# Performance work log

Hardware: AMD Instinct MI355X
Metric: run time of the kernel (lower is better)

The kernel has to match this reference:

```python
import jax, jax.numpy as jnp
import numpy as np

B, LV, LS = 16, 512, 512
FEA_V, FEA_S = 2048, 768
D_MODEL, H, DK, DV = 1024, 16, 64, 64
EPS = 1e-6


def setup_inputs() -> dict:
    key = jax.random.key(0)
    ks = jax.random.split(key, 16)
    sc = lambda fan_in: 1.0 / np.sqrt(fan_in)
    return {
        "v": jax.random.normal(ks[0], (B, LV, FEA_V), jnp.float32),
        "s": jax.random.normal(ks[1], (B, LS, FEA_S), jnp.float32),
        "W_lv": jax.random.normal(ks[2], (FEA_V, D_MODEL), jnp.float32) * sc(FEA_V),
        "b_lv": jnp.zeros((D_MODEL,), jnp.float32),
        "W_ls": jax.random.normal(ks[3], (FEA_S, D_MODEL), jnp.float32) * sc(FEA_S),
        "b_ls": jnp.zeros((D_MODEL,), jnp.float32),
        "pos_v": jax.random.normal(ks[4], (1, LV, D_MODEL), jnp.float32),
        "pos_s": jax.random.normal(ks[5], (1, LS, D_MODEL), jnp.float32),
        "W_q": jax.random.normal(ks[6], (D_MODEL, H * DK), jnp.float32) * sc(D_MODEL),
        "b_q": jnp.zeros((H * DK,), jnp.float32),
        "W_k": jax.random.normal(ks[7], (D_MODEL, H * DK), jnp.float32) * sc(D_MODEL),
        "b_k": jnp.zeros((H * DK,), jnp.float32),
        "W_v": jax.random.normal(ks[8], (D_MODEL, H * DV), jnp.float32) * sc(D_MODEL),
        "b_v": jnp.zeros((H * DV,), jnp.float32),
        "W_p": jax.random.normal(ks[9], (H * DV, D_MODEL), jnp.float32) * sc(H * DV),
        "b_p": jnp.zeros((D_MODEL,), jnp.float32),
        "ln_gamma": jnp.ones((D_MODEL,), jnp.float32),
        "ln_beta": jnp.zeros((D_MODEL,), jnp.float32),
        "v_len": LV,
        "s_len": LS,
    }


def _layer_norm(x, gamma, beta):
    mu = jnp.mean(x, axis=-1, keepdims=True)
    var = jnp.var(x, axis=-1, keepdims=True)
    return gamma * (x - mu) / jnp.sqrt(var + EPS) + beta


def reference(v, s, W_lv, b_lv, W_ls, b_ls, pos_v, pos_s, W_q, b_q, W_k, b_k,
              W_v, b_v, W_p, b_p, ln_gamma, ln_beta, v_len, s_len):
    b_size = v.shape[0]
    # input projections + ReLU (dropout is identity at eval)
    v = jax.nn.relu(v @ W_lv + b_lv)  # [B, LV, D]
    s = jax.nn.relu(s @ W_ls + b_ls)  # [B, LS, D]
    # positional embedding add (pos=True)
    residual_v = v + pos_v[:, : v.shape[1], :]
    # QKV projections; note the original unpack `q_v, k_s, k_s = ...`
    # overwrites the key with the VALUE projection of s, so both key and
    # value in attention are v_s (the W_v projection of s). W_k output is
    # computed in torch but discarded.
    q = (v @ W_q + b_q).reshape(b_size, -1, H, DK).transpose(0, 2, 1, 3)   # [B,H,LV,DK]
    _k = (s @ W_k + b_k)  # computed then discarded, kept for faithfulness
    vs = (s @ W_v + b_v).reshape(b_size, -1, H, DV).transpose(0, 2, 1, 3)  # [B,H,LS,DV]
    scores = jnp.einsum("bhqd,bhkd->bhqk", q, vs) / jnp.sqrt(jnp.float32(DK))
    attn = jax.nn.softmax(scores, axis=-1)
    context = jnp.einsum("bhqk,bhkd->bhqd", attn, vs)  # [B,H,LV,DV]
    context = context.transpose(0, 2, 1, 3).reshape(b_size, -1, H * DV)
    output_v = context @ W_p + b_p  # dropout identity at eval
    return _layer_norm(residual_v + output_v, ln_gamma, ln_beta)
```

## Files before the change

### kernel.cpp

```cpp
#include <hip/hip_runtime.h>

typedef unsigned short u16;
typedef unsigned int   u32;

using bf16x8 = __attribute__((ext_vector_type(8))) short;
using f32x4  = __attribute__((ext_vector_type(4))) float;

#define MFMA16(a, b, c) __builtin_amdgcn_mfma_f32_16x16x32_bf16((a), (b), (c), 0, 0, 0)

__device__ __forceinline__ u16 f2bf(float f) {
  union { float f; u32 u; } x; x.f = f;
  u32 r = x.u + 0x7fffu + ((x.u >> 16) & 1u);
  return (u16)(r >> 16);
}

__device__ __forceinline__ float bf2f(u16 v) {
  union { u32 u; float f; } x; x.u = ((u32)v) << 16;
  return x.f;
}

__device__ __forceinline__ u32 cvtpk(float lo, float hi) {
  u32 r;
  asm("v_cvt_pk_bf16_f32 %0, %1, %2" : "=v"(r) : "v"(lo), "v"(hi));
  return r;
}

__device__ __forceinline__ void gl2lds16(const void* g, void* l) {
  __builtin_amdgcn_global_load_lds(
      (const __attribute__((address_space(1))) u32*)g,
      (__attribute__((address_space(3))) u32*)l, 16, 0, 0);
}

__global__ __launch_bounds__(256) void cvt_all(const float* __restrict__ v_in,
                                               u16* __restrict__ v_bf,
                                               const float* __restrict__ s_in,
                                               u16* __restrict__ s_bf) {
  long i = (long)blockIdx.x * 256 + threadIdx.x;
  const float* in;
  u16* out;
  if (i < 2097152) {
    in = v_in + i * 8;
    out = v_bf + i * 8;
  } else {
    long j = i - 2097152;
    in = s_in + j * 8;
    out = s_bf + j * 8;
  }
  const float4* p = (const float4*)in;
  float4 a = p[0], b = p[1];
  uint4 pk;
  pk.x = cvtpk(a.x, a.y);
  pk.y = cvtpk(a.z, a.w);
  pk.z = cvtpk(b.x, b.y);
  pk.w = cvtpk(b.z, b.w);
  *(uint4*)out = pk;
}

__device__ __forceinline__ void wt_body(const float* __restrict__ W,
                                        u16* __restrict__ Wt, int K, int N,
                                        int bid, u16 (*t)[66]) {
  int tilesN = N >> 6;
  int k0 = (bid / tilesN) << 6;
  int n0 = (bid % tilesN) << 6;
  int tid = threadIdx.x;
  int c4 = (tid & 15) * 4, r16 = tid >> 4;
#pragma unroll
  for (int p = 0; p < 4; ++p) {
    int row = r16 + p * 16;
    float4 f = *(const float4*)(W + (size_t)(k0 + row) * N + n0 + c4);
    t[row][c4 + 0] = f2bf(f.x);
    t[row][c4 + 1] = f2bf(f.y);
    t[row][c4 + 2] = f2bf(f.z);
    t[row][c4 + 3] = f2bf(f.w);
  }
  __syncthreads();
  int c8 = (tid & 7) * 8, r32 = tid >> 3;
#pragma unroll
  for (int p = 0; p < 2; ++p) {
    int n = r32 + p * 32;
    u16 tmp[8] __attribute__((aligned(16)));
#pragma unroll
    for (int e = 0; e < 8; ++e) tmp[e] = t[c8 + e][n];
    *(uint4*)(Wt + (size_t)(n0 + n) * K + k0 + c8) = *(uint4*)tmp;
  }
}

__global__ __launch_bounds__(256) void wt_all(
    const float* W_lv, u16* Wlv_t, const float* W_ls, u16* Wls_t,
    const float* W_q, u16* Wq_t, const float* W_v, u16* Wv_t,
    const float* W_p, u16* Wp_t) {
  __shared__ u16 t[64][66];
  int b = (int)blockIdx.x;
  if (b < 512)        wt_body(W_lv, Wlv_t, 2048, 1024, b, t);
  else if (b < 704)   wt_body(W_ls, Wls_t, 768, 1024, b - 512, t);
  else if (b < 960)   wt_body(W_q, Wq_t, 1024, 1024, b - 704, t);
  else if (b < 1216)  wt_body(W_v, Wv_t, 1024, 1024, b - 960, t);
  else                wt_body(W_p, Wp_t, 1024, 1024, b - 1216, t);
}

struct GArgs {
  const u16* A; const u16* Bt; const float* bias;
  u16* outb; float* outf; u16* outt;
  const u16* add0b; const float* add1;
  int M, N, K;
};

template <int MODE>
__device__ __forceinline__ void gemm_body(u16* sAs, u16* sBs, const GArgs g,
                                          int orig, int nwg) {
  const u16* A = g.A;
  const u16* Bt = g.Bt;
  int N = g.N, K = g.K;
  int tilesN = N >> 7;
  int cpx = nwg >> 3;
  int wg = (orig & 7) * cpx + (orig >> 3);
  int tm = wg / tilesN, tn = wg % tilesN;
  int m0 = tm << 7, n0 = tn << 7;
  int tid = threadIdx.x, w = tid >> 6, l = tid & 63;
  int wm = (w >> 2) << 6, wn = (w & 3) << 5;
  int c16 = l & 15, hi = l >> 4, g16 = hi * 16;

  f32x4 acc[4][2];
#pragma unroll
  for (int i = 0; i < 4; ++i)
#pragma unroll
    for (int j = 0; j < 2; ++j) acc[i][j] = (f32x4){0.f, 0.f, 0.f, 0.f};

  auto STAGE = [&](int kt, int buf) {
    const u16* Ab = A + (size_t)m0 * K + kt * 64;
    const u16* Bb = Bt + (size_t)n0 * K + kt * 64;
#pragma unroll
    for (int p = 0; p < 2; ++p) {
      int lin = p * 8192 + tid * 16;
      int row = lin >> 7;
      int cb = (lin & 127) ^ ((row & 7) << 4);
      int base = lin & ~1023;
      gl2lds16(Ab + (size_t)row * K + (cb >> 1), (char*)sAs + buf * 16384 + base);
      gl2lds16(Bb + (size_t)row * K + (cb >> 1), (char*)sBs + buf * 16384 + base);
    }
  };

  auto COMPUTE = [&](int buf) {
#pragma unroll
    for (int kk = 0; kk < 2; ++kk) {
      bf16x8 af[4], bfr[2];
#pragma unroll
      for (int i = 0; i < 4; ++i) {
        int ar = wm + i * 16 + c16;
        af[i] = *(const bf16x8*)((const char*)sAs + buf * 16384 + ar * 128 +
                                 ((kk * 64 + g16) ^ ((ar & 7) << 4)));
      }
#pragma unroll
      for (int j = 0; j < 2; ++j) {
        int br = wn + j * 16 + c16;
        bfr[j] = *(const bf16x8*)((const char*)sBs + buf * 16384 + br * 128 +
                                  ((kk * 64 + g16) ^ ((br & 7) << 4)));
      }
#pragma unroll
      for (int i = 0; i < 4; ++i)
#pragma unroll
        for (int j = 0; j < 2; ++j) acc[i][j] = MFMA16(af[i], bfr[j], acc[i][j]);
    }
  };

  int nk = K >> 6;
  STAGE(0, 0);
  int cur = 0;
  for (int kt = 0; kt < nk; ++kt) {
    if (kt + 1 < nk) {
      STAGE(kt + 1, cur ^ 1);
      __builtin_amdgcn_sched_barrier(0);
      asm volatile("s_waitcnt vmcnt(4)" ::: "memory");
    } else {
      asm volatile("s_waitcnt vmcnt(0)" ::: "memory");
    }
    __builtin_amdgcn_s_barrier();
    __builtin_amdgcn_sched_barrier(0);
    COMPUTE(cur);
    __builtin_amdgcn_sched_barrier(0);
    __builtin_amdgcn_s_barrier();
    cur ^= 1;
  }

#pragma unroll
  for (int i = 0; i < 4; ++i) {
#pragma unroll
    for (int j = 0; j < 2; ++j) {
      float vv[4];
      int gn = n0 + wn + j * 16 + c16;
#pragma unroll
      for (int r = 0; r < 4; ++r) vv[r] = acc[i][j][r] + g.bias[gn];
      int gm0 = m0 + wm + i * 16 + hi * 4;
      if (MODE == 0) {
#pragma unroll
        for (int r = 0; r < 4; ++r)
          g.outb[(size_t)(gm0 + r) * N + gn] = f2bf(fmaxf(vv[r], 0.f));
      } else if (MODE == 2 || MODE == 4) {
        int hh = gn >> 6, dk = gn & 63, bb2 = gm0 >> 9, ll2 = gm0 & 511;
#pragma unroll
        for (int r = 0; r < 4; ++r)
          g.outb[(((size_t)bb2 * 16 + hh) * 512 + ll2 + r) * 64 + dk] = f2bf(vv[r]);
        if (MODE == 4) {
          uint2 tw;
          tw.x = cvtpk(vv[0], vv[1]);
          tw.y = cvtpk(vv[2], vv[3]);
          *(uint2*)(g.outt + (((size_t)bb2 * 16 + hh) * 64 + dk) * 512 + ll2) = tw;
        }
      } else {
#pragma unroll
        for (int r = 0; r < 4; ++r) {
          int gm = gm0 + r;
          float v = vv[r] + bf2f(g.add0b[(size_t)gm * N + gn]) +
                    g.add1[(size_t)(gm & 511) * N + gn];
          g.outf[(size_t)gm * N + gn] = v;
        }
      }
    }
  }
}

template <int MODEA, int MODEB>
__global__ __launch_bounds__(512) void gemm_pair(GArgs ga, GArgs gb) {
  __shared__ u16 sA[2 * 8192];
  __shared__ u16 sB[2 * 8192];
  int b = (int)blockIdx.x;
  if (b < 512) gemm_body<MODEA>(sA, sB, ga, b, 512);
  else         gemm_body<MODEB>(sA, sB, gb, b - 512, 512);
}

template <int MODE>
__global__ __launch_bounds__(512) void gemm_single(GArgs g) {
  __shared__ u16 sA[2 * 8192];
  __shared__ u16 sB[2 * 8192];
  gemm_body<MODE>(sA, sB, g, (int)blockIdx.x, (int)gridDim.x);
}

__global__ __launch_bounds__(512) void attn_kernel(const u16* __restrict__ q,
                                                   const u16* __restrict__ kv,
                                                   const u16* __restrict__ kvT,
                                                   u16* __restrict__ ctx) {
  __shared__ u16 sK[2][4096];
  __shared__ u16 sVT[2][4096];
  __shared__ u16 sP[8192];

  int orig = (int)blockIdx.x;
  int r = (orig & 7) * 128 + (orig >> 3);
  int bh = r >> 2, qt = r & 3;
  int b = bh >> 4, h = bh & 15;
  int tid = threadIdx.x, w = tid >> 6, l = tid & 63;
  int c16 = l & 15, hi = l >> 4, g16 = hi * 16;
  int swzq = (c16 & 7) << 4;

  const u16* qbase = q + (size_t)bh * 32768 + (size_t)qt * 8192;
#pragma unroll
  for (int j = 0; j < 2; ++j) {
    int chunk = w * 2 + j;
    int lin = chunk * 1024 + l * 16;
    int row = lin >> 7;
    int cb = (lin & 127) ^ ((row & 7) << 4);
    gl2lds16(qbase + (size_t)row * 64 + (cb >> 1), (char*)sP + chunk * 1024);
  }
  {
    const u16* kb = kv + (size_t)bh * 32768;
    const u16* vb = kvT + (size_t)bh * 32768;
    int lin = w * 1024 + l * 16;
    int row = lin >> 7;
    int cb = (lin & 127) ^ ((row & 7) << 4);
    gl2lds16(kb + (size_t)row * 64 + (cb >> 1), (char*)sK[0] + w * 1024);
    gl2lds16(vb + (size_t)row * 512 + (cb >> 1), (char*)sVT[0] + w * 1024);
  }
  __syncthreads();

  const char* sQrow = (const char*)sP + (w * 16 + c16) * 128;
  bf16x8 qf0 = *(const bf16x8*)(sQrow + ((0 + g16) ^ swzq));
  bf16x8 qf1 = *(const bf16x8*)(sQrow + ((64 + g16) ^ swzq));

  char* sPw = (char*)sP + w * 2048;
  f32x4 of[4];
#pragma unroll
  for (int n = 0; n < 4; ++n) of[n] = (f32x4){0.f, 0.f, 0.f, 0.f};
  float m_run = -1e30f, l_run = 0.f;

  for (int c = 0; c < 8; ++c) {
    int cur = c & 1;
    if (c < 7) {
      const u16* kb = kv + (size_t)bh * 32768 + (size_t)(c + 1) * 4096;
      const u16* vb = kvT + (size_t)bh * 32768 + (c + 1) * 64;
      int lin = w * 1024 + l * 16;
      int row = lin >> 7;
      int cb = (lin & 127) ^ ((row & 7) << 4);
      gl2lds16(kb + (size_t)row * 64 + (cb >> 1), (char*)sK[cur ^ 1] + w * 1024);
      gl2lds16(vb + (size_t)row * 512 + (cb >> 1), (char*)sVT[cur ^ 1] + w * 1024);
    }
    const char* kbuf = (const char*)sK[cur];
    const char* vtbuf = (const char*)sVT[cur];

    f32x4 sf[4];
#pragma unroll
    for (int n = 0; n < 4; ++n) {
      const char* krow = kbuf + (n * 16 + c16) * 128;
      bf16x8 k0 = *(const bf16x8*)(krow + (g16 ^ swzq));
      bf16x8 k1 = *(const bf16x8*)(krow + ((64 + g16) ^ swzq));
      f32x4 z = (f32x4){0.f, 0.f, 0.f, 0.f};
      z = MFMA16(k0, qf0, z);
      z = MFMA16(k1, qf1, z);
      sf[n] = z;
    }

    float pmax = -1e30f;
#pragma unroll
    for (int n = 0; n < 4; ++n)
#pragma unroll
      for (int rr = 0; rr < 4; ++rr) {
        sf[n][rr] *= 0.125f;
        pmax = fmaxf(pmax, sf[n][rr]);
      }
    pmax = fmaxf(pmax, __shfl_xor(pmax, 16));
    pmax = fmaxf(pmax, __shfl_xor(pmax, 32));
    float mnew = fmaxf(m_run, pmax);
    float corr = __expf(m_run - mnew);
    float psum = 0.f;
#pragma unroll
    for (int n = 0; n < 4; ++n)
#pragma unroll
      for (int rr = 0; rr < 4; ++rr) {
        float p = __expf(sf[n][rr] - mnew);
        sf[n][rr] = p;
        psum += p;
      }
    psum += __shfl_xor(psum, 16);
    psum += __shfl_xor(psum, 32);
    l_run = l_run * corr + psum;
    m_run = mnew;
#pragma unroll
    for (int n = 0; n < 4; ++n)
#pragma unroll
      for (int rr = 0; rr < 4; ++rr) of[n][rr] *= corr;

#pragma unroll
    for (int n = 0; n < 4; ++n) {
      uint2 pw;
      pw.x = cvtpk(sf[n][0], sf[n][1]);
      pw.y = cvtpk(sf[n][2], sf[n][3]);
      *(uint2*)(sPw + c16 * 128 + ((n * 32 + hi * 8) ^ swzq)) = pw;
    }

    bf16x8 pf0 = *(const bf16x8*)(sPw + c16 * 128 + (g16 ^ swzq));
    bf16x8 pf1 = *(const bf16x8*)(sPw + c16 * 128 + ((64 + g16) ^ swzq));
#pragma unroll
    for (int n = 0; n < 4; ++n) {
      const char* vrow = vtbuf + (n * 16 + c16) * 128;
      bf16x8 v0 = *(const bf16x8*)(vrow + (g16 ^ swzq));
      bf16x8 v1 = *(const bf16x8*)(vrow + ((64 + g16) ^ swzq));
      of[n] = MFMA16(v0, pf0, of[n]);
      of[n] = MFMA16(v1, pf1, of[n]);
    }
    __syncthreads();
  }

  float inv = 1.0f / l_run;
  int grow = qt * 128 + w * 16 + c16;
  u16* obase = ctx + (size_t)(b * 512 + grow) * 1024 + h * 64;
#pragma unroll
  for (int n = 0; n < 4; ++n) {
    uint2 ow;
    ow.x = cvtpk(of[n][0] * inv, of[n][1] * inv);
    ow.y = cvtpk(of[n][2] * inv, of[n][3] * inv);
    *(uint2*)(obase + n * 16 + hi * 4) = ow;
  }
}

__global__ __launch_bounds__(256) void ln_kernel(float* __restrict__ x,
                                                 const float* __restrict__ gamma,
                                                 const float* __restrict__ beta) {
  __shared__ float red[4];
  __shared__ float red2[4];
  int row = blockIdx.x, tid = threadIdx.x;
  float4 v = *(float4*)(x + (size_t)row * 1024 + tid * 4);
  float s = v.x + v.y + v.z + v.w;
#pragma unroll
  for (int d = 1; d < 64; d <<= 1) s += __shfl_xor(s, d);
  if ((tid & 63) == 0) red[tid >> 6] = s;
  __syncthreads();
  float mu = (red[0] + red[1] + red[2] + red[3]) * (1.0f / 1024.0f);
  float d0 = v.x - mu, d1 = v.y - mu, d2 = v.z - mu, d3 = v.w - mu;
  float qq = d0 * d0 + d1 * d1 + d2 * d2 + d3 * d3;
#pragma unroll
  for (int d = 1; d < 64; d <<= 1) qq += __shfl_xor(qq, d);
  if ((tid & 63) == 0) red2[tid >> 6] = qq;
  __syncthreads();
  float var = (red2[0] + red2[1] + red2[2] + red2[3]) * (1.0f / 1024.0f);
  float rstd = rsqrtf(var + 1e-6f);
  float4 g = *(const float4*)(gamma + tid * 4);
  float4 bb = *(const float4*)(beta + tid * 4);
  v.x = g.x * d0 * rstd + bb.x;
  v.y = g.y * d1 * rstd + bb.y;
  v.z = g.z * d2 * rstd + bb.z;
  v.w = g.w * d3 * rstd + bb.w;
  *(float4*)(x + (size_t)row * 1024 + tid * 4) = v;
}

extern "C" void kernel_launch(void* const* d_in, const int* in_sizes, int n_in,
                              void* d_out, int out_size, void* d_ws, size_t ws_size,
                              hipStream_t stream) {
  (void)in_sizes; (void)n_in; (void)out_size; (void)ws_size;
  const float* v_in  = (const float*)d_in[0];
  const float* s_in  = (const float*)d_in[1];
  const float* W_lv  = (const float*)d_in[2];
  const float* b_lv  = (const float*)d_in[3];
  const float* W_ls  = (const float*)d_in[4];
  const float* b_ls  = (const float*)d_in[5];
  const float* pos_v = (const float*)d_in[6];
  const float* W_q   = (const float*)d_in[8];
  const float* b_q   = (const float*)d_in[9];
  const float* W_v   = (const float*)d_in[12];
  const float* b_v   = (const float*)d_in[13];
  const float* W_p   = (const float*)d_in[14];
  const float* b_p   = (const float*)d_in[15];
  const float* gamma = (const float*)d_in[16];
  const float* beta  = (const float*)d_in[17];
  float* out = (float*)d_out;

  char* ws = (char*)d_ws;
  size_t off = 0;
  auto alloc = [&](size_t bytes) {
    char* p = ws + off;
    off += (bytes + 255) & ~(size_t)255;
    return p;
  };
  u16* v_bf     = (u16*)alloc(33554432);
  u16* s_bf     = (u16*)alloc(12582912);
  u16* Wlv_t    = (u16*)alloc(4194304);
  u16* Wls_t    = (u16*)alloc(1572864);
  u16* Wq_t     = (u16*)alloc(2097152);
  u16* Wv_t     = (u16*)alloc(2097152);
  u16* Wp_t     = (u16*)alloc(2097152);
  u16* vproj_bf = (u16*)alloc(16777216);
  u16* sproj_bf = (u16*)alloc(16777216);
  u16* q_bf     = (u16*)alloc(16777216);
  u16* vs_bf    = (u16*)alloc(16777216);
  u16* vsT_bf   = (u16*)alloc(16777216);
  u16* ctx_bf   = (u16*)alloc(16777216);

  cvt_all<<<11264, 256, 0, stream>>>(v_in, v_bf, s_in, s_bf);
  wt_all<<<1472, 256, 0, stream>>>(W_lv, Wlv_t, W_ls, Wls_t, W_q, Wq_t,
                                   W_v, Wv_t, W_p, Wp_t);

  GArgs av  = {v_bf, Wlv_t, b_lv, vproj_bf, nullptr, nullptr, nullptr, nullptr,
               8192, 1024, 2048};
  GArgs as  = {s_bf, Wls_t, b_ls, sproj_bf, nullptr, nullptr, nullptr, nullptr,
               8192, 1024, 768};
  GArgs aq  = {vproj_bf, Wq_t, b_q, q_bf, nullptr, nullptr, nullptr, nullptr,
               8192, 1024, 1024};
  GArgs avs = {sproj_bf, Wv_t, b_v, vs_bf, nullptr, vsT_bf, nullptr, nullptr,
               8192, 1024, 1024};
  GArgs ao  = {ctx_bf, Wp_t, b_p, nullptr, out, nullptr, vproj_bf, pos_v,
               8192, 1024, 1024};

  gemm_pair<0, 0><<<1024, 512, 0, stream>>>(av, as);
  gemm_pair<2, 4><<<1024, 512, 0, stream>>>(aq, avs);
  attn_kernel<<<1024, 512, 0, stream>>>(q_bf, vs_bf, vsT_bf, ctx_bf);
  gemm_single<3><<<512, 512, 0, stream>>>(ao);
  ln_kernel<<<8192, 256, 0, stream>>>(out, gamma, beta);
}
```

Baseline: 210.2 us.

## Merge prologue kernels, fold softmax scale into Q, defer rescaling, fuse residual into LN

Merges the input cast and weight transpose into one prologue launch. The 1/sqrt(dk) scale moves into the Q projection epilogue, and the online softmax skips the max update and rescale when the new max exceeds the running max by no more than 8 across the wave. The output projection now writes bf16 instead of fp32 with residual adds, and a fused LayerNorm reads the bf16 projection, the bf16 residual and pos to build the sum. This cuts launches, per-tile exp/scale work and fp32 traffic, but stores the pre-LN projection output in bf16, which loses some precision.

New measurement: 198.7 us. -5.5%, faster.

```diff
diff --git a/kernel.cpp b/kernel.cpp
--- a/kernel.cpp
+++ b/kernel.cpp
@@ -29,31 +29,6 @@
   __builtin_amdgcn_global_load_lds(
       (const __attribute__((address_space(1))) u32*)g,
       (__attribute__((address_space(3))) u32*)l, 16, 0, 0);
-}
-
-__global__ __launch_bounds__(256) void cvt_all(const float* __restrict__ v_in,
-                                               u16* __restrict__ v_bf,
-                                               const float* __restrict__ s_in,
-                                               u16* __restrict__ s_bf) {
-  long i = (long)blockIdx.x * 256 + threadIdx.x;
-  const float* in;
-  u16* out;
-  if (i < 2097152) {
-    in = v_in + i * 8;
-    out = v_bf + i * 8;
-  } else {
-    long j = i - 2097152;
-    in = s_in + j * 8;
-    out = s_bf + j * 8;
-  }
-  const float4* p = (const float4*)in;
-  float4 a = p[0], b = p[1];
-  uint4 pk;
-  pk.x = cvtpk(a.x, a.y);
-  pk.y = cvtpk(a.z, a.w);
-  pk.z = cvtpk(b.x, b.y);
-  pk.w = cvtpk(b.z, b.w);
-  *(uint4*)out = pk;
 }
 
 __device__ __forceinline__ void wt_body(const float* __restrict__ W,
@@ -85,17 +60,41 @@
   }
 }
 
-__global__ __launch_bounds__(256) void wt_all(
+__global__ __launch_bounds__(256) void prologue_all(
+    const float* v_in, u16* v_bf, const float* s_in, u16* s_bf,
     const float* W_lv, u16* Wlv_t, const float* W_ls, u16* Wls_t,
     const float* W_q, u16* Wq_t, const float* W_v, u16* Wv_t,
     const float* W_p, u16* Wp_t) {
   __shared__ u16 t[64][66];
-  int b = (int)blockIdx.x;
-  if (b < 512)        wt_body(W_lv, Wlv_t, 2048, 1024, b, t);
-  else if (b < 704)   wt_body(W_ls, Wls_t, 768, 1024, b - 512, t);
-  else if (b < 960)   wt_body(W_q, Wq_t, 1024, 1024, b - 704, t);
-  else if (b < 1216)  wt_body(W_v, Wv_t, 1024, 1024, b - 960, t);
-  else                wt_body(W_p, Wp_t, 1024, 1024, b - 1216, t);
+  long blk = (long)blockIdx.x;
+  if (blk < 11264) {
+    long i = blk * 256 + threadIdx.x;
+    const float* in;
+    u16* out;
+    if (i < 2097152) {
+      in = v_in + i * 8;
+      out = v_bf + i * 8;
+    } else {
+      long j = i - 2097152;
+      in = s_in + j * 8;
+      out = s_bf + j * 8;
+    }
+    const float4* p = (const float4*)in;
+    float4 a = p[0], b = p[1];
+    uint4 pk;
+    pk.x = cvtpk(a.x, a.y);
+    pk.y = cvtpk(a.z, a.w);
+    pk.z = cvtpk(b.x, b.y);
+    pk.w = cvtpk(b.z, b.w);
+    *(uint4*)out = pk;
+  } else {
+    int b = (int)blk - 11264;
+    if (b < 512)        wt_body(W_lv, Wlv_t, 2048, 1024, b, t);
+    else if (b < 704)   wt_body(W_ls, Wls_t, 768, 1024, b - 512, t);
+    else if (b < 960)   wt_body(W_q, Wq_t, 1024, 1024, b - 704, t);
+    else if (b < 1216)  wt_body(W_v, Wv_t, 1024, 1024, b - 960, t);
+    else                wt_body(W_p, Wp_t, 1024, 1024, b - 1216, t);
+  }
 }
 
 struct GArgs {
@@ -195,24 +194,22 @@
 #pragma unroll
         for (int r = 0; r < 4; ++r)
           g.outb[(size_t)(gm0 + r) * N + gn] = f2bf(fmaxf(vv[r], 0.f));
+      } else if (MODE == 5) {
+#pragma unroll
+        for (int r = 0; r < 4; ++r)
+          g.outb[(size_t)(gm0 + r) * N + gn] = f2bf(vv[r]);
       } else if (MODE == 2 || MODE == 4) {
         int hh = gn >> 6, dk = gn & 63, bb2 = gm0 >> 9, ll2 = gm0 & 511;
 #pragma unroll
-        for (int r = 0; r < 4; ++r)
-          g.outb[(((size_t)bb2 * 16 + hh) * 512 + ll2 + r) * 64 + dk] = f2bf(vv[r]);
+        for (int r = 0; r < 4; ++r) {
+          float ov = (MODE == 2) ? vv[r] * 0.125f : vv[r];
+          g.outb[(((size_t)bb2 * 16 + hh) * 512 + ll2 + r) * 64 + dk] = f2bf(ov);
+        }
         if (MODE == 4) {
           uint2 tw;
           tw.x = cvtpk(vv[0], vv[1]);
           tw.y = cvtpk(vv[2], vv[3]);
           *(uint2*)(g.outt + (((size_t)bb2 * 16 + hh) * 64 + dk) * 512 + ll2) = tw;
-        }
-      } else {
-#pragma unroll
-        for (int r = 0; r < 4; ++r) {
-          int gm = gm0 + r;
-          float v = vv[r] + bf2f(g.add0b[(size_t)gm * N + gn]) +
-                    g.add1[(size_t)(gm & 511) * N + gn];
-          g.outf[(size_t)gm * N + gn] = v;
         }
       }
     }
@@ -311,31 +308,33 @@
 #pragma unroll
     for (int n = 0; n < 4; ++n)
 #pragma unroll
-      for (int rr = 0; rr < 4; ++rr) {
-        sf[n][rr] *= 0.125f;
-        pmax = fmaxf(pmax, sf[n][rr]);
-      }
+      for (int rr = 0; rr < 4; ++rr) pmax = fmaxf(pmax, sf[n][rr]);
     pmax = fmaxf(pmax, __shfl_xor(pmax, 16));
     pmax = fmaxf(pmax, __shfl_xor(pmax, 32));
-    float mnew = fmaxf(m_run, pmax);
-    float corr = __expf(m_run - mnew);
+
+    bool defer = __all(pmax - m_run <= 8.f) != 0;
+    float mnew = defer ? m_run : fmaxf(m_run, pmax);
+    if (!defer) {
+      float corr = __expf(m_run - mnew);
+#pragma unroll
+      for (int n = 0; n < 4; ++n)
+#pragma unroll
+        for (int rr = 0; rr < 4; ++rr) of[n][rr] *= corr;
+      l_run *= corr;
+      m_run = mnew;
+    }
     float psum = 0.f;
 #pragma unroll
     for (int n = 0; n < 4; ++n)
 #pragma unroll
       for (int rr = 0; rr < 4; ++rr) {
-        float p = __expf(sf[n][rr] - mnew);
+        float p = __expf(sf[n][rr] - m_run);
         sf[n][rr] = p;
         psum += p;
       }
     psum += __shfl_xor(psum, 16);
     psum += __shfl_xor(psum, 32);
-    l_run = l_run * corr + psum;
-    m_run = mnew;
-#pragma unroll
-    for (int n = 0; n < 4; ++n)
-#pragma unroll
-      for (int rr = 0; rr < 4; ++rr) of[n][rr] *= corr;
+    l_run += psum;
 
 #pragma unroll
     for (int n = 0; n < 4; ++n) {
@@ -370,20 +369,30 @@
   }
 }
 
-__global__ __launch_bounds__(256) void ln_kernel(float* __restrict__ x,
-                                                 const float* __restrict__ gamma,
-                                                 const float* __restrict__ beta) {
+__global__ __launch_bounds__(256) void ln_fused(const u16* __restrict__ gbf,
+                                                const u16* __restrict__ resid,
+                                                const float* __restrict__ pos,
+                                                const float* __restrict__ gamma,
+                                                const float* __restrict__ beta,
+                                                float* __restrict__ out) {
   __shared__ float red[4];
   __shared__ float red2[4];
   int row = blockIdx.x, tid = threadIdx.x;
-  float4 v = *(float4*)(x + (size_t)row * 1024 + tid * 4);
-  float s = v.x + v.y + v.z + v.w;
+  size_t base = (size_t)row * 1024 + tid * 4;
+  uint2 gg = *(const uint2*)(gbf + base);
+  uint2 rr = *(const uint2*)(resid + base);
+  float4 pp = *(const float4*)(pos + (size_t)(row & 511) * 1024 + tid * 4);
+  float x0 = bf2f((u16)(gg.x & 0xffff)) + bf2f((u16)(rr.x & 0xffff)) + pp.x;
+  float x1 = bf2f((u16)(gg.x >> 16))    + bf2f((u16)(rr.x >> 16))    + pp.y;
+  float x2 = bf2f((u16)(gg.y & 0xffff)) + bf2f((u16)(rr.y & 0xffff)) + pp.z;
+  float x3 = bf2f((u16)(gg.y >> 16))    + bf2f((u16)(rr.y >> 16))    + pp.w;
+  float s = x0 + x1 + x2 + x3;
 #pragma unroll
   for (int d = 1; d < 64; d <<= 1) s += __shfl_xor(s, d);
   if ((tid & 63) == 0) red[tid >> 6] = s;
   __syncthreads();
   float mu = (red[0] + red[1] + red[2] + red[3]) * (1.0f / 1024.0f);
-  float d0 = v.x - mu, d1 = v.y - mu, d2 = v.z - mu, d3 = v.w - mu;
+  float d0 = x0 - mu, d1 = x1 - mu, d2 = x2 - mu, d3 = x3 - mu;
   float qq = d0 * d0 + d1 * d1 + d2 * d2 + d3 * d3;
 #pragma unroll
   for (int d = 1; d < 64; d <<= 1) qq += __shfl_xor(qq, d);
@@ -391,13 +400,14 @@
   __syncthreads();
   float var = (red2[0] + red2[1] + red2[2] + red2[3]) * (1.0f / 1024.0f);
   float rstd = rsqrtf(var + 1e-6f);
-  float4 g = *(const float4*)(gamma + tid * 4);
-  float4 bb = *(const float4*)(beta + tid * 4);
-  v.x = g.x * d0 * rstd + bb.x;
-  v.y = g.y * d1 * rstd + bb.y;
-  v.z = g.z * d2 * rstd + bb.z;
-  v.w = g.w * d3 * rstd + bb.w;
-  *(float4*)(x + (size_t)row * 1024 + tid * 4) = v;
+  float4 g4 = *(const float4*)(gamma + tid * 4);
+  float4 b4 = *(const float4*)(beta + tid * 4);
+  float4 o;
+  o.x = g4.x * d0 * rstd + b4.x;
+  o.y = g4.y * d1 * rstd + b4.y;
+  o.z = g4.z * d2 * rstd + b4.z;
+  o.w = g4.w * d3 * rstd + b4.w;
+  *(float4*)(out + base) = o;
 }
 
 extern "C" void kernel_launch(void* const* d_in, const int* in_sizes, int n_in,
@@ -441,10 +451,11 @@
   u16* vs_bf    = (u16*)alloc(16777216);
   u16* vsT_bf   = (u16*)alloc(16777216);
   u16* ctx_bf   = (u16*)alloc(16777216);
-
-  cvt_all<<<11264, 256, 0, stream>>>(v_in, v_bf, s_in, s_bf);
-  wt_all<<<1472, 256, 0, stream>>>(W_lv, Wlv_t, W_ls, Wls_t, W_q, Wq_t,
-                                   W_v, Wv_t, W_p, Wp_t);
+  u16* oproj_bf = (u16*)alloc(16777216);
+
+  prologue_all<<<12736, 256, 0, stream>>>(v_in, v_bf, s_in, s_bf,
+                                          W_lv, Wlv_t, W_ls, Wls_t, W_q, Wq_t,
+                                          W_v, Wv_t, W_p, Wp_t);
 
   GArgs av  = {v_bf, Wlv_t, b_lv, vproj_bf, nullptr, nullptr, nullptr, nullptr,
                8192, 1024, 2048};
@@ -454,12 +465,12 @@
                8192, 1024, 1024};
   GArgs avs = {sproj_bf, Wv_t, b_v, vs_bf, nullptr, vsT_bf, nullptr, nullptr,
                8192, 1024, 1024};
-  GArgs ao  = {ctx_bf, Wp_t, b_p, nullptr, out, nullptr, vproj_bf, pos_v,
+  GArgs ao  = {ctx_bf, Wp_t, b_p, oproj_bf, nullptr, nullptr, nullptr, nullptr,
                8192, 1024, 1024};
 
   gemm_pair<0, 0><<<1024, 512, 0, stream>>>(av, as);
   gemm_pair<2, 4><<<1024, 512, 0, stream>>>(aq, avs);
   attn_kernel<<<1024, 512, 0, stream>>>(q_bf, vs_bf, vsT_bf, ctx_bf);
-  gemm_single<3><<<512, 512, 0, stream>>>(ao);
-  ln_kernel<<<8192, 256, 0, stream>>>(out, gamma, beta);
-}
+  gemm_single<5><<<512, 512, 0, stream>>>(ao);
+  ln_fused<<<8192, 256, 0, stream>>>(oproj_bf, vproj_bf, pos_v, gamma, beta, out);
+}
```
